# Kernel optimization log

Hardware: AMD Instinct MI355X
Metric: run time of the kernel (lower is better)

Reference implementation:

```python
import jax, jax.numpy as jnp
import numpy as np

INPUT_DIMS = 512
OUTPUT_DIMS = 512
DEGREE = 7
ALPHA = 1.0


def setup_inputs() -> dict:
    key = jax.random.key(0)
    k1, k2 = jax.random.split(key)
    x = jax.random.normal(k1, (16384, INPUT_DIMS), dtype=jnp.float32)
    std = 1.0 / (INPUT_DIMS * (DEGREE + 1))
    coeffs = jax.random.normal(k2, (INPUT_DIMS, OUTPUT_DIMS, DEGREE + 1), dtype=jnp.float32) * std
    return {"x": x, "gegenbauer_coeffs": coeffs}


def reference(x, gegenbauer_coeffs):
    # x: (B, I) -> tanh squashed into (-1, 1) domain of Gegenbauer polys
    x = jnp.tanh(x.reshape(-1, INPUT_DIMS))
    a = ALPHA
    polys = [jnp.ones_like(x)]
    if DEGREE > 0:
        polys.append(2.0 * a * x)
    # recurrence: C_{n+1} = (2(n+a) x C_n - (n+2a-1) C_{n-1}) / (n+1)
    for n in range(1, DEGREE):
        polys.append((2.0 * (n + a) * x * polys[n] - (n + 2.0 * a - 1.0) * polys[n - 1]) / (n + 1.0))
    g = jnp.stack(polys, axis=-1)  # (B, I, D+1)
    y = jnp.einsum('bid,iod->bo', g, gegenbauer_coeffs)
    return y.reshape(-1, OUTPUT_DIMS)
```

## Files before the change

### kernel.cpp

```cpp
#include <hip/hip_runtime.h>
#include <hip/hip_bf16.h>


#define I_DIM 512
#define O_DIM 512
#define NDEG 8
#define KH_ITERS 32
#define W_ELEMS (I_DIM * O_DIM * NDEG)

typedef __attribute__((ext_vector_type(8))) short s8v;
typedef __attribute__((ext_vector_type(4))) float f32x4;
typedef unsigned short u16;

__device__ __forceinline__ unsigned cvt_pk_bf16(float lo, float hi) {
    unsigned r;
    asm("v_cvt_pk_bf16_f32 %0, %1, %2" : "=v"(r) : "v"(lo), "v"(hi));
    return r;
}

__device__ __forceinline__ float fast_tanh(float v) {
    float e = __expf(v + v);
    float r = __builtin_amdgcn_rcpf(e + 1.0f);
    return 1.0f - (r + r);
}

__device__ __forceinline__ s8v feat_frag(float xv) {
    const float t  = fast_tanh(xv);
    const float t2 = t + t;
    const float c1 = t2;
    const float c2 = t2 * c1 - 1.0f;
    const float c3 = t2 * c2 - c1;
    const float c4 = t2 * c3 - c2;
    const float c5 = t2 * c4 - c3;
    const float c6 = t2 * c5 - c4;
    const float c7 = t2 * c6 - c5;
    union { s8v s; unsigned u[4]; } pk;
    pk.u[0] = cvt_pk_bf16(1.0f, c1);
    pk.u[1] = cvt_pk_bf16(c2, c3);
    pk.u[2] = cvt_pk_bf16(c4, c5);
    pk.u[3] = cvt_pk_bf16(c6, c7);
    return pk.s;
}

extern "C" __global__ __launch_bounds__(256)
void cvt_w(const float* __restrict__ cf, u16* __restrict__ wbf) {
    const size_t idx = ((size_t)blockIdx.x * 256 + threadIdx.x) * 4;
    const float4 v = *reinterpret_cast<const float4*>(cf + idx);
    unsigned* dst = reinterpret_cast<unsigned*>(wbf + idx);
    dst[0] = cvt_pk_bf16(v.x, v.y);
    dst[1] = cvt_pk_bf16(v.z, v.w);
}

template <bool PRECONV>
__global__ __launch_bounds__(256, 4)
void gegen_gemm(const float* __restrict__ x,
                const float* __restrict__ cf,
                const u16* __restrict__ wbf,
                float* __restrict__ out)
{
    __shared__ float smem[4096];

    const int tid  = threadIdx.x;
    const int lane = tid & 63;
    const int wave = tid >> 6;
    const int m4   = wave & 1;
    const int kh   = wave >> 1;
    const int fm   = lane & 15;
    const int fq   = lane >> 4;

    const int bm0 = blockIdx.x * 128 + m4 * 64;
    const int bn0 = blockIdx.y * 64;
    const int kbase = kh * (KH_ITERS * 8);

    const float* xrow = x + (size_t)(bm0 + lane) * I_DIM + kbase;
    float* xslot = &smem[wave * 1024];

    f32x4 acc[4][4];
#pragma unroll
    for (int a = 0; a < 4; ++a)
#pragma unroll
        for (int b = 0; b < 4; ++b)
            acc[a][b] = (f32x4){0.0f, 0.0f, 0.0f, 0.0f};

    {
        const float4 xa = *reinterpret_cast<const float4*>(xrow);
        const float4 xb = *reinterpret_cast<const float4*>(xrow + 4);
        *reinterpret_cast<f32x4*>(&xslot[lane * 8])     = (f32x4){xa.x, xa.y, xa.z, xa.w};
        *reinterpret_cast<f32x4*>(&xslot[lane * 8 + 4]) = (f32x4){xb.x, xb.y, xb.z, xb.w};
    }

    for (int it = 0; it < KH_ITERS; ++it) {
        const int g8   = kbase + it * 8;
        const int buf  = (it & 1) * 512;
        const int nbuf = buf ^ 512;

        s8v bfr0[4], bfr1[4];
        if (PRECONV) {
            const u16* wb0 = wbf + ((size_t)(g8 + fq) * O_DIM + bn0 + fm) * NDEG;
            const u16* wb1 = wb0 + (size_t)4 * O_DIM * NDEG;
#pragma unroll
            for (int tn = 0; tn < 4; ++tn)
                bfr0[tn] = *reinterpret_cast<const s8v*>(wb0 + tn * 16 * NDEG);
#pragma unroll
            for (int tn = 0; tn < 4; ++tn)
                bfr1[tn] = *reinterpret_cast<const s8v*>(wb1 + tn * 16 * NDEG);
        } else {
            const float* wb0 = cf + ((size_t)(g8 + fq) * O_DIM + bn0 + fm) * NDEG;
            const float* wb1 = wb0 + (size_t)4 * O_DIM * NDEG;
#pragma unroll
            for (int tn = 0; tn < 4; ++tn) {
                const float4 w0 = reinterpret_cast<const float4*>(wb0 + tn * 16 * NDEG)[0];
                const float4 w1 = reinterpret_cast<const float4*>(wb0 + tn * 16 * NDEG)[1];
                union { s8v s; unsigned u[4]; } pk;
                pk.u[0] = cvt_pk_bf16(w0.x, w0.y);
                pk.u[1] = cvt_pk_bf16(w0.z, w0.w);
                pk.u[2] = cvt_pk_bf16(w1.x, w1.y);
                pk.u[3] = cvt_pk_bf16(w1.z, w1.w);
                bfr0[tn] = pk.s;
            }
#pragma unroll
            for (int tn = 0; tn < 4; ++tn) {
                const float4 w0 = reinterpret_cast<const float4*>(wb1 + tn * 16 * NDEG)[0];
                const float4 w1 = reinterpret_cast<const float4*>(wb1 + tn * 16 * NDEG)[1];
                union { s8v s; unsigned u[4]; } pk;
                pk.u[0] = cvt_pk_bf16(w0.x, w0.y);
                pk.u[1] = cvt_pk_bf16(w0.z, w0.w);
                pk.u[2] = cvt_pk_bf16(w1.x, w1.y);
                pk.u[3] = cvt_pk_bf16(w1.z, w1.w);
                bfr1[tn] = pk.s;
            }
        }

        float4 xa2, xb2;
        const bool more = (it + 1 < KH_ITERS);
        if (more) {
            xa2 = *reinterpret_cast<const float4*>(xrow + (it + 1) * 8);
            xb2 = *reinterpret_cast<const float4*>(xrow + (it + 1) * 8 + 4);
        }

        asm volatile("s_waitcnt lgkmcnt(0)" ::: "memory");

        s8v afr[4];
#pragma unroll
        for (int tm = 0; tm < 4; ++tm)
            afr[tm] = feat_frag(xslot[buf + (tm * 16 + fm) * 8 + fq]);

        __builtin_amdgcn_s_setprio(1);
#pragma unroll
        for (int tm = 0; tm < 4; ++tm)
#pragma unroll
            for (int tn = 0; tn < 4; ++tn)
                acc[tm][tn] = __builtin_amdgcn_mfma_f32_16x16x32_bf16(
                    afr[tm], bfr0[tn], acc[tm][tn], 0, 0, 0);
        __builtin_amdgcn_s_setprio(0);

#pragma unroll
        for (int tm = 0; tm < 4; ++tm)
            afr[tm] = feat_frag(xslot[buf + (tm * 16 + fm) * 8 + 4 + fq]);

        __builtin_amdgcn_s_setprio(1);
#pragma unroll
        for (int tm = 0; tm < 4; ++tm)
#pragma unroll
            for (int tn = 0; tn < 4; ++tn)
                acc[tm][tn] = __builtin_amdgcn_mfma_f32_16x16x32_bf16(
                    afr[tm], bfr1[tn], acc[tm][tn], 0, 0, 0);
        __builtin_amdgcn_s_setprio(0);

        if (more) {
            *reinterpret_cast<f32x4*>(&xslot[nbuf + lane * 8])     = (f32x4){xa2.x, xa2.y, xa2.z, xa2.w};
            *reinterpret_cast<f32x4*>(&xslot[nbuf + lane * 8 + 4]) = (f32x4){xb2.x, xb2.y, xb2.z, xb2.w};
        }
    }

    __syncthreads();
#pragma unroll
    for (int tm = 0; tm < 4; ++tm) {
        if (kh == 1) {
#pragma unroll
            for (int tn = 0; tn < 4; ++tn)
#pragma unroll
                for (int r = 0; r < 4; ++r)
                    smem[m4 * 1024 + (fq * 4 + r) * 64 + tn * 16 + fm] = acc[tm][tn][r];
        }
        __syncthreads();
        if (kh == 0) {
#pragma unroll
            for (int tn = 0; tn < 4; ++tn) {
                const int row = bm0 + tm * 16 + fq * 4;
                const int col = bn0 + tn * 16 + fm;
#pragma unroll
                for (int r = 0; r < 4; ++r)
                    out[(size_t)(row + r) * O_DIM + col] =
                        acc[tm][tn][r] + smem[m4 * 1024 + (fq * 4 + r) * 64 + tn * 16 + fm];
            }
        }
        __syncthreads();
    }
}

extern "C" void kernel_launch(void* const* d_in, const int* in_sizes, int n_in,
                              void* d_out, int out_size, void* d_ws, size_t ws_size,
                              hipStream_t stream) {
    const float* x  = (const float*)d_in[0];
    const float* cf = (const float*)d_in[1];
    float* out = (float*)d_out;
    const int M = in_sizes[0] / I_DIM;
    dim3 grid(M / 128, O_DIM / 64);
    dim3 block(256, 1, 1);

    if (ws_size >= (size_t)W_ELEMS * sizeof(u16)) {
        u16* wbf = (u16*)d_ws;
        cvt_w<<<W_ELEMS / 1024, 256, 0, stream>>>(cf, wbf);
        gegen_gemm<true><<<grid, block, 0, stream>>>(x, cf, wbf, out);
    } else {
        gegen_gemm<false><<<grid, block, 0, stream>>>(x, cf, nullptr, out);
    }
}
```

Before: 178.2 us.

## Switch to 32x32x16 MFMA with a 128-wide N tile per block

Replaces the 16x16x32 bf16 MFMA tiling with 32x32x16 MFMAs and doubles the output-column tile per block to 128. The A-side features are computed once per k-slice and reused across four N subtiles, which halves the number of blocks. The x staging in LDS is padded to a stride of 10 floats to reduce bank conflicts, and feature generation is software-pipelined between MFMA groups. The larger tile needs more registers for the accumulators and B fragments, so occupancy drops to 2 blocks per SIMD, and the epilogue now takes more syncthreads rounds.

```diff
diff --git a/kernel.cpp b/kernel.cpp
--- a/kernel.cpp
+++ b/kernel.cpp
@@ -9,7 +9,7 @@
 #define W_ELEMS (I_DIM * O_DIM * NDEG)
 
 typedef __attribute__((ext_vector_type(8))) short s8v;
-typedef __attribute__((ext_vector_type(4))) float f32x4;
+typedef __attribute__((ext_vector_type(16))) float f32x16;
 typedef unsigned short u16;
 
 __device__ __forceinline__ unsigned cvt_pk_bf16(float lo, float hi) {
@@ -51,84 +51,83 @@
     dst[1] = cvt_pk_bf16(v.z, v.w);
 }
 
+__device__ __forceinline__ s8v ldb(const u16* p) {
+    return *reinterpret_cast<const s8v*>(p);
+}
+__device__ __forceinline__ s8v ldb_cvt(const float* p) {
+    const float4 w0 = reinterpret_cast<const float4*>(p)[0];
+    const float4 w1 = reinterpret_cast<const float4*>(p)[1];
+    union { s8v s; unsigned u[4]; } pk;
+    pk.u[0] = cvt_pk_bf16(w0.x, w0.y);
+    pk.u[1] = cvt_pk_bf16(w0.z, w0.w);
+    pk.u[2] = cvt_pk_bf16(w1.x, w1.y);
+    pk.u[3] = cvt_pk_bf16(w1.z, w1.w);
+    return pk.s;
+}
+
 template <bool PRECONV>
-__global__ __launch_bounds__(256, 4)
+__global__ __launch_bounds__(256, 2)
 void gegen_gemm(const float* __restrict__ x,
                 const float* __restrict__ cf,
                 const u16* __restrict__ wbf,
                 float* __restrict__ out)
 {
-    __shared__ float smem[4096];
+    __shared__ float smem[5120];
 
     const int tid  = threadIdx.x;
     const int lane = tid & 63;
     const int wave = tid >> 6;
     const int m4   = wave & 1;
     const int kh   = wave >> 1;
-    const int fm   = lane & 15;
-    const int fq   = lane >> 4;
+    const int l31  = lane & 31;
+    const int l5   = lane >> 5;
 
     const int bm0 = blockIdx.x * 128 + m4 * 64;
-    const int bn0 = blockIdx.y * 64;
+    const int bn0 = blockIdx.y * 128;
     const int kbase = kh * (KH_ITERS * 8);
 
     const float* xrow = x + (size_t)(bm0 + lane) * I_DIM + kbase;
-    float* xslot = &smem[wave * 1024];
-
-    f32x4 acc[4][4];
-#pragma unroll
-    for (int a = 0; a < 4; ++a)
+    float* xslot = &smem[wave * 1280];
+
+    f32x16 acc[2][4];
+#pragma unroll
+    for (int a = 0; a < 2; ++a)
 #pragma unroll
         for (int b = 0; b < 4; ++b)
-            acc[a][b] = (f32x4){0.0f, 0.0f, 0.0f, 0.0f};
+#pragma unroll
+            for (int r = 0; r < 16; ++r)
+                acc[a][b][r] = 0.0f;
 
     {
         const float4 xa = *reinterpret_cast<const float4*>(xrow);
         const float4 xb = *reinterpret_cast<const float4*>(xrow + 4);
-        *reinterpret_cast<f32x4*>(&xslot[lane * 8])     = (f32x4){xa.x, xa.y, xa.z, xa.w};
-        *reinterpret_cast<f32x4*>(&xslot[lane * 8 + 4]) = (f32x4){xb.x, xb.y, xb.z, xb.w};
+        float* p = &xslot[lane * 10];
+        *reinterpret_cast<float2*>(p + 0) = make_float2(xa.x, xa.y);
+        *reinterpret_cast<float2*>(p + 2) = make_float2(xa.z, xa.w);
+        *reinterpret_cast<float2*>(p + 4) = make_float2(xb.x, xb.y);
+        *reinterpret_cast<float2*>(p + 6) = make_float2(xb.z, xb.w);
     }
 
     for (int it = 0; it < KH_ITERS; ++it) {
         const int g8   = kbase + it * 8;
-        const int buf  = (it & 1) * 512;
-        const int nbuf = buf ^ 512;
-
-        s8v bfr0[4], bfr1[4];
+        const int buf  = (it & 1) * 640;
+        const int nbuf = buf ^ 640;
+
+        s8v bfr[4][4];
         if (PRECONV) {
-            const u16* wb0 = wbf + ((size_t)(g8 + fq) * O_DIM + bn0 + fm) * NDEG;
-            const u16* wb1 = wb0 + (size_t)4 * O_DIM * NDEG;
-#pragma unroll
-            for (int tn = 0; tn < 4; ++tn)
-                bfr0[tn] = *reinterpret_cast<const s8v*>(wb0 + tn * 16 * NDEG);
-#pragma unroll
-            for (int tn = 0; tn < 4; ++tn)
-                bfr1[tn] = *reinterpret_cast<const s8v*>(wb1 + tn * 16 * NDEG);
+            const u16* wb = wbf + ((size_t)(g8 + l5) * O_DIM + bn0 + l31) * NDEG;
+#pragma unroll
+            for (int ks = 0; ks < 4; ++ks)
+#pragma unroll
+                for (int tn = 0; tn < 4; ++tn)
+                    bfr[ks][tn] = ldb(wb + ((size_t)ks * 2 * O_DIM + tn * 32) * NDEG);
         } else {
-            const float* wb0 = cf + ((size_t)(g8 + fq) * O_DIM + bn0 + fm) * NDEG;
-            const float* wb1 = wb0 + (size_t)4 * O_DIM * NDEG;
-#pragma unroll
-            for (int tn = 0; tn < 4; ++tn) {
-                const float4 w0 = reinterpret_cast<const float4*>(wb0 + tn * 16 * NDEG)[0];
-                const float4 w1 = reinterpret_cast<const float4*>(wb0 + tn * 16 * NDEG)[1];
-                union { s8v s; unsigned u[4]; } pk;
-                pk.u[0] = cvt_pk_bf16(w0.x, w0.y);
-                pk.u[1] = cvt_pk_bf16(w0.z, w0.w);
-                pk.u[2] = cvt_pk_bf16(w1.x, w1.y);
-                pk.u[3] = cvt_pk_bf16(w1.z, w1.w);
-                bfr0[tn] = pk.s;
-            }
-#pragma unroll
-            for (int tn = 0; tn < 4; ++tn) {
-                const float4 w0 = reinterpret_cast<const float4*>(wb1 + tn * 16 * NDEG)[0];
-                const float4 w1 = reinterpret_cast<const float4*>(wb1 + tn * 16 * NDEG)[1];
-                union { s8v s; unsigned u[4]; } pk;
-                pk.u[0] = cvt_pk_bf16(w0.x, w0.y);
-                pk.u[1] = cvt_pk_bf16(w0.z, w0.w);
-                pk.u[2] = cvt_pk_bf16(w1.x, w1.y);
-                pk.u[3] = cvt_pk_bf16(w1.z, w1.w);
-                bfr1[tn] = pk.s;
-            }
+            const float* wb = cf + ((size_t)(g8 + l5) * O_DIM + bn0 + l31) * NDEG;
+#pragma unroll
+            for (int ks = 0; ks < 4; ++ks)
+#pragma unroll
+                for (int tn = 0; tn < 4; ++tn)
+                    bfr[ks][tn] = ldb_cvt(wb + ((size_t)ks * 2 * O_DIM + tn * 32) * NDEG);
         }
 
         float4 xa2, xb2;
@@ -140,62 +139,91 @@
 
         asm volatile("s_waitcnt lgkmcnt(0)" ::: "memory");
 
-        s8v afr[4];
-#pragma unroll
-        for (int tm = 0; tm < 4; ++tm)
-            afr[tm] = feat_frag(xslot[buf + (tm * 16 + fm) * 8 + fq]);
-
-        __builtin_amdgcn_s_setprio(1);
-#pragma unroll
-        for (int tm = 0; tm < 4; ++tm)
-#pragma unroll
-            for (int tn = 0; tn < 4; ++tn)
-                acc[tm][tn] = __builtin_amdgcn_mfma_f32_16x16x32_bf16(
-                    afr[tm], bfr0[tn], acc[tm][tn], 0, 0, 0);
-        __builtin_amdgcn_s_setprio(0);
-
-#pragma unroll
-        for (int tm = 0; tm < 4; ++tm)
-            afr[tm] = feat_frag(xslot[buf + (tm * 16 + fm) * 8 + 4 + fq]);
-
-        __builtin_amdgcn_s_setprio(1);
-#pragma unroll
-        for (int tm = 0; tm < 4; ++tm)
-#pragma unroll
-            for (int tn = 0; tn < 4; ++tn)
-                acc[tm][tn] = __builtin_amdgcn_mfma_f32_16x16x32_bf16(
-                    afr[tm], bfr1[tn], acc[tm][tn], 0, 0, 0);
-        __builtin_amdgcn_s_setprio(0);
+        const int bt0 = buf + l31 * 10 + l5;
+        const int bt1 = buf + (32 + l31) * 10 + l5;
+
+        s8v aA = feat_frag(xslot[bt0]);
+        s8v aB = feat_frag(xslot[bt1]);
+        s8v nA, nB;
+
+        nA = feat_frag(xslot[bt0 + 2]);
+        nB = feat_frag(xslot[bt1 + 2]);
+        __builtin_amdgcn_s_setprio(1);
+#pragma unroll
+        for (int tn = 0; tn < 4; ++tn)
+            acc[0][tn] = __builtin_amdgcn_mfma_f32_32x32x16_bf16(aA, bfr[0][tn], acc[0][tn], 0, 0, 0);
+#pragma unroll
+        for (int tn = 0; tn < 4; ++tn)
+            acc[1][tn] = __builtin_amdgcn_mfma_f32_32x32x16_bf16(aB, bfr[0][tn], acc[1][tn], 0, 0, 0);
+        __builtin_amdgcn_s_setprio(0);
+        aA = nA; aB = nB;
+
+        nA = feat_frag(xslot[bt0 + 4]);
+        nB = feat_frag(xslot[bt1 + 4]);
+        __builtin_amdgcn_s_setprio(1);
+#pragma unroll
+        for (int tn = 0; tn < 4; ++tn)
+            acc[0][tn] = __builtin_amdgcn_mfma_f32_32x32x16_bf16(aA, bfr[1][tn], acc[0][tn], 0, 0, 0);
+#pragma unroll
+        for (int tn = 0; tn < 4; ++tn)
+            acc[1][tn] = __builtin_amdgcn_mfma_f32_32x32x16_bf16(aB, bfr[1][tn], acc[1][tn], 0, 0, 0);
+        __builtin_amdgcn_s_setprio(0);
+        aA = nA; aB = nB;
+
+        nA = feat_frag(xslot[bt0 + 6]);
+        nB = feat_frag(xslot[bt1 + 6]);
+        __builtin_amdgcn_s_setprio(1);
+#pragma unroll
+        for (int tn = 0; tn < 4; ++tn)
+            acc[0][tn] = __builtin_amdgcn_mfma_f32_32x32x16_bf16(aA, bfr[2][tn], acc[0][tn], 0, 0, 0);
+#pragma unroll
+        for (int tn = 0; tn < 4; ++tn)
+            acc[1][tn] = __builtin_amdgcn_mfma_f32_32x32x16_bf16(aB, bfr[2][tn], acc[1][tn], 0, 0, 0);
+        __builtin_amdgcn_s_setprio(0);
+        aA = nA; aB = nB;
 
         if (more) {
-            *reinterpret_cast<f32x4*>(&xslot[nbuf + lane * 8])     = (f32x4){xa2.x, xa2.y, xa2.z, xa2.w};
-            *reinterpret_cast<f32x4*>(&xslot[nbuf + lane * 8 + 4]) = (f32x4){xb2.x, xb2.y, xb2.z, xb2.w};
-        }
+            float* p = &xslot[nbuf + lane * 10];
+            *reinterpret_cast<float2*>(p + 0) = make_float2(xa2.x, xa2.y);
+            *reinterpret_cast<float2*>(p + 2) = make_float2(xa2.z, xa2.w);
+            *reinterpret_cast<float2*>(p + 4) = make_float2(xb2.x, xb2.y);
+            *reinterpret_cast<float2*>(p + 6) = make_float2(xb2.z, xb2.w);
+        }
+        __builtin_amdgcn_s_setprio(1);
+#pragma unroll
+        for (int tn = 0; tn < 4; ++tn)
+            acc[0][tn] = __builtin_amdgcn_mfma_f32_32x32x16_bf16(aA, bfr[3][tn], acc[0][tn], 0, 0, 0);
+#pragma unroll
+        for (int tn = 0; tn < 4; ++tn)
+            acc[1][tn] = __builtin_amdgcn_mfma_f32_32x32x16_bf16(aB, bfr[3][tn], acc[1][tn], 0, 0, 0);
+        __builtin_amdgcn_s_setprio(0);
     }
 
     __syncthreads();
 #pragma unroll
-    for (int tm = 0; tm < 4; ++tm) {
-        if (kh == 1) {
-#pragma unroll
-            for (int tn = 0; tn < 4; ++tn)
-#pragma unroll
-                for (int r = 0; r < 4; ++r)
-                    smem[m4 * 1024 + (fq * 4 + r) * 64 + tn * 16 + fm] = acc[tm][tn][r];
-        }
-        __syncthreads();
-        if (kh == 0) {
-#pragma unroll
-            for (int tn = 0; tn < 4; ++tn) {
-                const int row = bm0 + tm * 16 + fq * 4;
-                const int col = bn0 + tn * 16 + fm;
-#pragma unroll
-                for (int r = 0; r < 4; ++r)
-                    out[(size_t)(row + r) * O_DIM + col] =
-                        acc[tm][tn][r] + smem[m4 * 1024 + (fq * 4 + r) * 64 + tn * 16 + fm];
+    for (int tm = 0; tm < 2; ++tm) {
+#pragma unroll
+        for (int tn = 0; tn < 4; ++tn) {
+            if (kh == 1) {
+#pragma unroll
+                for (int r = 0; r < 16; ++r) {
+                    const int rowoff = (r & 3) + 8 * (r >> 2) + 4 * l5;
+                    smem[m4 * 1024 + rowoff * 32 + l31] = acc[tm][tn][r];
+                }
             }
-        }
-        __syncthreads();
+            __syncthreads();
+            if (kh == 0) {
+#pragma unroll
+                for (int r = 0; r < 16; ++r) {
+                    const int rowoff = (r & 3) + 8 * (r >> 2) + 4 * l5;
+                    const int row = bm0 + tm * 32 + rowoff;
+                    const int col = bn0 + tn * 32 + l31;
+                    out[(size_t)row * O_DIM + col] =
+                        acc[tm][tn][r] + smem[m4 * 1024 + rowoff * 32 + l31];
+                }
+            }
+            __syncthreads();
+        }
     }
 }
 
@@ -206,7 +234,7 @@
     const float* cf = (const float*)d_in[1];
     float* out = (float*)d_out;
     const int M = in_sizes[0] / I_DIM;
-    dim3 grid(M / 128, O_DIM / 64);
+    dim3 grid(M / 128, O_DIM / 128);
     dim3 block(256, 1, 1);
 
     if (ws_size >= (size_t)W_ELEMS * sizeof(u16)) {
```

Measured after the change: 158.4 us. 1.13x faster.
